# Kernel optimization log

Hardware: AMD Instinct MI355X
Metric: run time of the kernel (lower is better)

The kernel has to match this reference:

```python
import jax, jax.numpy as jnp
import numpy as np

GROUPS = 32
EPS = 1e-6


def group_norm(x, gamma, beta):
    # x: [b, c, d, h, w]
    b, c, d, h, w = x.shape
    xg = x.reshape(b, GROUPS, c // GROUPS, d, h, w)
    mean = xg.mean(axis=(2, 3, 4, 5), keepdims=True)
    var = xg.var(axis=(2, 3, 4, 5), keepdims=True)
    xn = ((xg - mean) * jax.lax.rsqrt(var + EPS)).reshape(b, c, d, h, w)
    return xn * gamma[None, :, None, None, None] + beta[None, :, None, None, None]


def conv1x1(x, w, bias):
    # 1x1x1 Conv3d == channel matmul. x: [b,c,d,h,w], w: [out,in]
    return jnp.einsum('bcdhw,oc->bodhw', x, w) + bias[None, :, None, None, None]


def setup_inputs() -> dict:
    key = jax.random.key(0)
    ks = jax.random.split(key, 6)
    C = 256
    x = jax.random.normal(ks[0], (4, C, 16, 16, 16), dtype=jnp.float32)
    s = 1.0 / np.sqrt(C)
    return {
        'x': x,
        'gn_gamma': jnp.ones((C,), jnp.float32),
        'gn_beta': jnp.zeros((C,), jnp.float32),
        'wq': jax.random.normal(ks[1], (C, C), jnp.float32) * s,
        'bq': jnp.zeros((C,), jnp.float32),
        'wk': jax.random.normal(ks[2], (C, C), jnp.float32) * s,
        'bk': jnp.zeros((C,), jnp.float32),
        'wv': jax.random.normal(ks[3], (C, C), jnp.float32) * s,
        'bv': jnp.zeros((C,), jnp.float32),
        'wo': jax.random.normal(ks[4], (C, C), jnp.float32) * s,
        'bo': jnp.zeros((C,), jnp.float32),
    }


def reference(x, gn_gamma, gn_beta, wq, bq, wk, bk, wv, bv, wo, bo):
    b, c, d, h, w = x.shape
    n = d * h * w
    hn = group_norm(x, gn_gamma, gn_beta)
    q = conv1x1(hn, wq, bq).reshape(b, c, n)  # [b,c,n]
    k = conv1x1(hn, wk, bk).reshape(b, c, n)
    v = conv1x1(hn, wv, bv).reshape(b, c, n)
    # NOTE: no 1/sqrt(c) scaling, faithful to source
    scores = jnp.einsum('bci,bcj->bij', q, k)          # [b,n,n]
    attn = jax.nn.softmax(scores, axis=-1)
    out = jnp.einsum('bij,bcj->bci', attn, v)           # [b,c,n]
    out = out.reshape(b, c, d, h, w)
    out = conv1x1(out, wo, bo)
    return x + out
```

## Files before the change

### kernel.cpp

```cpp
#include <hip/hip_runtime.h>
#include <hip/hip_bf16.h>

#define C_ 256
#define N_ 4096
#define B_ 4
#define NG_ 32
#define CPG_ 8
#define SPLITS 4
#define GPARTS 8
#define JT_PER (N_ / 32 / SPLITS)

typedef _Float16 f16;
typedef __attribute__((ext_vector_type(8))) _Float16 f16v8;
typedef __attribute__((ext_vector_type(2))) __fp16 fp16v2;
typedef __attribute__((ext_vector_type(4))) float f32x4;
typedef __attribute__((ext_vector_type(2))) unsigned int u32x2;
typedef __attribute__((ext_vector_type(4))) unsigned int u32x4;

__device__ __forceinline__ f16v8 ldh(const f16* p) {
    return *reinterpret_cast<const f16v8*>(p);
}
__device__ __forceinline__ f32x4 mfma16(f16v8 a, f16v8 b, f32x4 c) {
    return __builtin_amdgcn_mfma_f32_16x16x32_f16(a, b, c, 0, 0, 0);
}
__device__ __forceinline__ unsigned int pkh(float a, float b) {
    fp16v2 t = __builtin_amdgcn_cvt_pkrtz(a, b);
    return __builtin_bit_cast(unsigned int, t);
}
__device__ __forceinline__ u32x2 plchain(unsigned int x, unsigned int y) {
    u32x2 t = __builtin_amdgcn_permlane32_swap(x, y, false, false);
    return __builtin_amdgcn_permlane16_swap(t.x, t.y, false, false);
}

__global__ __launch_bounds__(256) void conv_w_kernel(
    const float* __restrict__ wq, const float* __restrict__ wk,
    const float* __restrict__ wv, const float* __restrict__ wo,
    f16* __restrict__ wq16, f16* __restrict__ wk16,
    f16* __restrict__ wv16, f16* __restrict__ wo16)
{
    int idx = blockIdx.x * 256 + threadIdx.x;
    wq16[idx] = (f16)wq[idx];
    wk16[idx] = (f16)wk[idx];
    wv16[idx] = (f16)wv[idx];
    wo16[idx] = (f16)wo[idx];
}

__global__ __launch_bounds__(256) void gn_stats_kernel(
    const float* __restrict__ x, float2* __restrict__ psums)
{
    int idx = blockIdx.x;
    int part = idx & (GPARTS - 1);
    int bg = idx >> 3;
    const float4* xv = (const float4*)(x + (size_t)bg * (CPG_ * N_)
                                         + (size_t)part * (CPG_ * N_ / GPARTS));
    int tid = threadIdx.x;
    float s = 0.f, s2 = 0.f;
    #pragma unroll
    for (int i = 0; i < CPG_ * N_ / GPARTS / 4 / 256; i++) {
        float4 v = xv[i * 256 + tid];
        s  += v.x + v.y + v.z + v.w;
        s2 += v.x * v.x + v.y * v.y + v.z * v.z + v.w * v.w;
    }
    #pragma unroll
    for (int off = 32; off > 0; off >>= 1) {
        s  += __shfl_down(s, off);
        s2 += __shfl_down(s2, off);
    }
    __shared__ float rs[4], rs2[4];
    if ((tid & 63) == 0) { rs[tid >> 6] = s; rs2[tid >> 6] = s2; }
    __syncthreads();
    if (tid == 0)
        psums[idx] = make_float2(rs[0] + rs[1] + rs[2] + rs[3],
                                 rs2[0] + rs2[1] + rs2[2] + rs2[3]);
}

__global__ __launch_bounds__(256) void gn_apply_kernel(
    const float* __restrict__ x, const float2* __restrict__ psums,
    const float* __restrict__ gamma, const float* __restrict__ beta,
    f16* __restrict__ hn)
{
    int idx = blockIdx.x;
    int p2 = idx & 15;
    int bg = idx >> 4;
    int b = bg >> 5, g = bg & 31;
    float S = 0.f, S2 = 0.f;
    #pragma unroll
    for (int s = 0; s < GPARTS; s++) {
        float2 ps = psums[bg * GPARTS + s];
        S += ps.x; S2 += ps.y;
    }
    float mean = S / (float)(CPG_ * N_);
    float rstd = rsqrtf(S2 / (float)(CPG_ * N_) - mean * mean + 1e-6f);
    int i = p2 * 256 + threadIdx.x;
    const float* xp = x + (size_t)(b * C_ + g * CPG_) * N_;
    f16v8 H;
    #pragma unroll
    for (int cc = 0; cc < CPG_; cc++) {
        float ga = gamma[g * CPG_ + cc] * rstd;
        float be = beta[g * CPG_ + cc];
        H[cc] = (f16)((xp[(size_t)cc * N_ + i] - mean) * ga + be);
    }
    *reinterpret_cast<f16v8*>(hn + (size_t)(b * N_ + i) * C_ + g * CPG_) = H;
}

__global__ __launch_bounds__(256) void proj_qk_kernel(
    const f16* __restrict__ hn, const f16* __restrict__ wq16,
    const f16* __restrict__ wk16, const float* __restrict__ bq,
    const float* __restrict__ bk, f16* __restrict__ qo, f16* __restrict__ ko)
{
    int it = blockIdx.x, b = blockIdx.y, z = blockIdx.z;
    int which = z >> 1, ochalf = z & 1;
    const f16* wgt = which ? wk16 : wq16;
    const float* bias = which ? bk : bq;
    f16* outp = which ? ko : qo;
    int tid = threadIdx.x, w = tid >> 6, l = tid & 63;
    int l15 = l & 15, lhi = l >> 4;
    int i0 = it * 64 + w * 16;
    size_t arow = (size_t)(b * N_ + i0 + l15) * C_ + lhi * 8;
    f16v8 af[8];
    #pragma unroll
    for (int kk = 0; kk < 8; kk++) af[kk] = ldh(hn + arow + kk * 32);
    for (int oc = ochalf * 8; oc < ochalf * 8 + 8; oc++) {
        f32x4 acc = {0.f, 0.f, 0.f, 0.f};
        size_t wrow = (size_t)(oc * 16 + l15) * C_ + lhi * 8;
        #pragma unroll
        for (int kk = 0; kk < 8; kk++)
            acc = mfma16(af[kk], ldh(wgt + wrow + kk * 32), acc);
        float bia = bias[oc * 16 + l15];
        #pragma unroll
        for (int r = 0; r < 4; r++)
            outp[(size_t)(b * N_ + i0 + lhi * 4 + r) * C_ + oc * 16 + l15] =
                (f16)(acc[r] + bia);
    }
}

__global__ __launch_bounds__(256) void proj_v_kernel(
    const f16* __restrict__ hn, const f16* __restrict__ wv16,
    const float* __restrict__ bv, f16* __restrict__ vT)
{
    int it = blockIdx.x, b = blockIdx.y;
    int tid = threadIdx.x, w = tid >> 6, l = tid & 63;
    int l15 = l & 15, lhi = l >> 4;
    int o0 = w * 64, i0 = it * 32;
    f32x4 acc[4][2];
    #pragma unroll
    for (int mc = 0; mc < 4; mc++)
        #pragma unroll
        for (int nc = 0; nc < 2; nc++) acc[mc][nc] = (f32x4){0.f, 0.f, 0.f, 0.f};
    for (int kk = 0; kk < 8; kk++) {
        f16v8 af[4], bfv[2];
        #pragma unroll
        for (int mc = 0; mc < 4; mc++)
            af[mc] = ldh(wv16 + (size_t)(o0 + mc * 16 + l15) * C_ + kk * 32 + lhi * 8);
        #pragma unroll
        for (int nc = 0; nc < 2; nc++)
            bfv[nc] = ldh(hn + (size_t)(b * N_ + i0 + nc * 16 + l15) * C_ + kk * 32 + lhi * 8);
        #pragma unroll
        for (int mc = 0; mc < 4; mc++)
            #pragma unroll
            for (int nc = 0; nc < 2; nc++)
                acc[mc][nc] = mfma16(af[mc], bfv[nc], acc[mc][nc]);
    }
    #pragma unroll
    for (int mc = 0; mc < 4; mc++) {
        float bia[4];
        #pragma unroll
        for (int r = 0; r < 4; r++) bia[r] = bv[o0 + mc * 16 + lhi * 4 + r];
        #pragma unroll
        for (int nc = 0; nc < 2; nc++)
            #pragma unroll
            for (int r = 0; r < 4; r++) {
                int o = o0 + mc * 16 + lhi * 4 + r;
                int i = i0 + nc * 16 + l15;
                vT[(size_t)(b * C_ + o) * N_ + i] = (f16)(acc[mc][nc][r] + bia[r]);
            }
    }
}

__device__ __forceinline__ void stage_k(const f16* kbase, f16* dst, int j0,
                                        int w, int l) {
    #pragma unroll
    for (int rd = 0; rd < 4; rd++) {
        int cb = (rd * 4 + w) * 64;
        int mc = cb + l;
        int row = mc >> 5;
        int xoff = ((mc & 31) << 4) ^ ((row & 7) << 4);
        const f16* gsrc = kbase + (size_t)(j0 + row) * C_ + (xoff >> 1);
        __builtin_amdgcn_global_load_lds(
            (const __attribute__((address_space(1))) void*)gsrc,
            (__attribute__((address_space(3))) void*)(dst + (size_t)cb * 8),
            16, 0, 0);
    }
}
__device__ __forceinline__ void stage_v(const f16* vbase, f16* dst, int j0,
                                        int w, int l) {
    int tid = w * 64 + l;
    int colu = ((l & 3) ^ ((l >> 3) & 3)) * 8;
    #pragma unroll
    for (int s = 0; s < 4; s++) {
        int cb = s * 256 + w * 64;
        const f16* gsrc = vbase + (size_t)(s * 64 + (tid >> 2)) * N_ + j0 + colu;
        __builtin_amdgcn_global_load_lds(
            (const __attribute__((address_space(1))) void*)gsrc,
            (__attribute__((address_space(3))) void*)(dst + (size_t)cb * 8),
            16, 0, 0);
    }
}

__global__ __launch_bounds__(256, 2) void flash_split_kernel(
    const f16* __restrict__ q, const f16* __restrict__ k,
    const f16* __restrict__ vT,
    f16* __restrict__ o0p, f16* __restrict__ o1p,
    f16* __restrict__ o2p, f16* __restrict__ o3p,
    float2* __restrict__ stats)
{
    int bi = blockIdx.x;
    int g = bi & 15;
    int it = bi >> 4;
    int b = g >> 2, split = g & 3;
    int tid = threadIdx.x, w = tid >> 6, l = tid & 63;
    int l15 = l & 15, lhi = l >> 4;
    int i0 = it * 128 + w * 32;
    int jt0 = split * JT_PER;
    __shared__ __align__(16) f16 kb[32][256];
    __shared__ __align__(16) f16 vb[2][256][32];

    const f16* kbase = k + (size_t)b * N_ * C_;
    const f16* vbase = vT + (size_t)b * C_ * N_;

    f16v8 qfA[8], qfB_[8];
    {
        size_t qrow0 = (size_t)(b * N_ + i0 + l15) * C_ + lhi * 8;
        size_t qrow1 = (size_t)(b * N_ + i0 + 16 + l15) * C_ + lhi * 8;
        #pragma unroll
        for (int kk = 0; kk < 8; kk++) {
            qfA[kk]  = ldh(q + qrow0 + kk * 32);
            qfB_[kk] = ldh(q + qrow1 + kk * 32);
        }
    }

    f32x4 oaccA[16], oaccB[16];
    #pragma unroll
    for (int cc = 0; cc < 16; cc++) {
        oaccA[cc] = (f32x4){0.f, 0.f, 0.f, 0.f};
        oaccB[cc] = (f32x4){0.f, 0.f, 0.f, 0.f};
    }
    float mA = -1e30f, rsA = 0.f;
    float mB = -1e30f, rsB = 0.f;

    int lhiV = lhi ^ ((l15 >> 1) & 3);

    stage_k(kbase, &kb[0][0], jt0 * 32, w, l);
    stage_v(vbase, &vb[0][0][0], jt0 * 32, w, l);
    __syncthreads();

    for (int jt = 0; jt < JT_PER; jt++) {
        int cur = jt & 1;
        int j0 = (jt0 + jt) * 32;

        if (jt + 1 < JT_PER)
            stage_v(vbase, &vb[cur ^ 1][0][0], j0 + 32, w, l);

        const char* kbc = (const char*)&kb[0][0];
        f32x4 sA0 = {0.f,0.f,0.f,0.f}, sA1 = {0.f,0.f,0.f,0.f};
        f32x4 sB0 = {0.f,0.f,0.f,0.f}, sB1 = {0.f,0.f,0.f,0.f};
        __builtin_amdgcn_s_setprio(1);
        #pragma unroll
        for (int kk = 0; kk < 8; kk++) {
            int row0 = l15, row1 = 16 + l15;
            int off0 = row0 * 512 + ((kk * 64 + lhi * 16) ^ ((row0 & 7) << 4));
            int off1 = row1 * 512 + ((kk * 64 + lhi * 16) ^ ((row1 & 7) << 4));
            f16v8 kf0 = *reinterpret_cast<const f16v8*>(kbc + off0);
            f16v8 kf1 = *reinterpret_cast<const f16v8*>(kbc + off1);
            sA0 = mfma16(kf0, qfA[kk], sA0);
            sA1 = mfma16(kf1, qfA[kk], sA1);
            sB0 = mfma16(kf0, qfB_[kk], sB0);
            sB1 = mfma16(kf1, qfB_[kk], sB1);
        }
        __builtin_amdgcn_s_setprio(0);

        __syncthreads();

        if (jt + 1 < JT_PER)
            stage_k(kbase, &kb[0][0], j0 + 32, w, l);

        float mtA = fmaxf(fmaxf(fmaxf(sA0[0], sA0[1]), fmaxf(sA0[2], sA0[3])),
                          fmaxf(fmaxf(sA1[0], sA1[1]), fmaxf(sA1[2], sA1[3])));
        float mtB = fmaxf(fmaxf(fmaxf(sB0[0], sB0[1]), fmaxf(sB0[2], sB0[3])),
                          fmaxf(fmaxf(sB1[0], sB1[1]), fmaxf(sB1[2], sB1[3])));
        mtA = fmaxf(mtA, __shfl_xor(mtA, 16));
        mtA = fmaxf(mtA, __shfl_xor(mtA, 32));
        mtB = fmaxf(mtB, __shfl_xor(mtB, 16));
        mtB = fmaxf(mtB, __shfl_xor(mtB, 32));
        if (!__all(mtA <= mA + 8.f && mtB <= mB + 8.f)) {
            float mnA = fmaxf(mA, mtA), mnB = fmaxf(mB, mtB);
            float scA = __expf(mA - mnA), scB = __expf(mB - mnB);
            mA = mnA; mB = mnB;
            rsA *= scA; rsB *= scB;
            #pragma unroll
            for (int cc = 0; cc < 16; cc++) {
                #pragma unroll
                for (int r = 0; r < 4; r++) {
                    oaccA[cc][r] *= scA;
                    oaccB[cc][r] *= scB;
                }
            }
        }
        float pA0[4], pA1[4], pB0[4], pB1[4];
        float lsA = 0.f, lsB = 0.f;
        #pragma unroll
        for (int r = 0; r < 4; r++) {
            pA0[r] = __expf(sA0[r] - mA);
            pA1[r] = __expf(sA1[r] - mA);
            pB0[r] = __expf(sB0[r] - mB);
            pB1[r] = __expf(sB1[r] - mB);
            lsA += pA0[r] + pA1[r];
            lsB += pB0[r] + pB1[r];
        }
        rsA += lsA; rsB += lsB;

        u32x2 rA01 = plchain(pkh(pA0[0], pA0[1]), pkh(pA1[0], pA1[1]));
        u32x2 rA23 = plchain(pkh(pA0[2], pA0[3]), pkh(pA1[2], pA1[3]));
        u32x4 fA = {rA01.x, rA23.x, rA01.y, rA23.y};
        f16v8 pfA = __builtin_bit_cast(f16v8, fA);
        u32x2 rB01 = plchain(pkh(pB0[0], pB0[1]), pkh(pB1[0], pB1[1]));
        u32x2 rB23 = plchain(pkh(pB0[2], pB0[3]), pkh(pB1[2], pB1[3]));
        u32x4 fB = {rB01.x, rB23.x, rB01.y, rB23.y};
        f16v8 pfB = __builtin_bit_cast(f16v8, fB);

        const f16* vbc = &vb[cur][0][0];
        __builtin_amdgcn_s_setprio(1);
        #pragma unroll
        for (int cc = 0; cc < 16; cc++) {
            f16v8 vf = ldh(vbc + (cc * 16 + l15) * 32 + lhiV * 8);
            oaccA[cc] = mfma16(vf, pfA, oaccA[cc]);
            oaccB[cc] = mfma16(vf, pfB, oaccB[cc]);
        }
        __builtin_amdgcn_s_setprio(0);

        __syncthreads();
    }

    rsA += __shfl_xor(rsA, 16); rsA += __shfl_xor(rsA, 32);
    rsB += __shfl_xor(rsB, 16); rsB += __shfl_xor(rsB, 32);
    float invA = 1.f / rsA, invB = 1.f / rsB;

    f16* op = (split == 0) ? o0p : (split == 1) ? o1p : (split == 2) ? o2p : o3p;
    size_t obaseA = (size_t)(b * N_ + i0 + l15) * C_;
    size_t obaseB = (size_t)(b * N_ + i0 + 16 + l15) * C_;
    #pragma unroll
    for (int cc = 0; cc < 16; cc++) {
        uint2 stA = {pkh(oaccA[cc][0] * invA, oaccA[cc][1] * invA),
                     pkh(oaccA[cc][2] * invA, oaccA[cc][3] * invA)};
        uint2 stB = {pkh(oaccB[cc][0] * invB, oaccB[cc][1] * invB),
                     pkh(oaccB[cc][2] * invB, oaccB[cc][3] * invB)};
        *reinterpret_cast<uint2*>(op + obaseA + cc * 16 + lhi * 4) = stA;
        *reinterpret_cast<uint2*>(op + obaseB + cc * 16 + lhi * 4) = stB;
    }
    if (lhi == 0) {
        stats[((size_t)split * B_ + b) * N_ + i0 + l15]      = make_float2(mA, rsA);
        stats[((size_t)split * B_ + b) * N_ + i0 + 16 + l15] = make_float2(mB, rsB);
    }
}

__global__ __launch_bounds__(256) void combine_kernel(
    const f16* __restrict__ o0p, const f16* __restrict__ o1p,
    const f16* __restrict__ o2p, const f16* __restrict__ o3p,
    const float2* __restrict__ stats, f16* __restrict__ att)
{
    int idx = blockIdx.x * 256 + threadIdx.x;
    int rowg = idx >> 5;
    int cof = (idx & 31) * 8;
    float2 st[SPLITS];
    float M = -1e30f;
    #pragma unroll
    for (int s = 0; s < SPLITS; s++) {
        st[s] = stats[(size_t)s * B_ * N_ + rowg];
        M = fmaxf(M, st[s].x);
    }
    float a[SPLITS], L = 0.f;
    #pragma unroll
    for (int s = 0; s < SPLITS; s++) {
        a[s] = st[s].y * __expf(st[s].x - M);
        L += a[s];
    }
    float inv = 1.f / L;
    size_t base = (size_t)rowg * C_ + cof;
    f16v8 v0 = ldh(o0p + base), v1 = ldh(o1p + base);
    f16v8 v2 = ldh(o2p + base), v3 = ldh(o3p + base);
    f16v8 o = v0 * (f16)(a[0] * inv) + v1 * (f16)(a[1] * inv)
            + v2 * (f16)(a[2] * inv) + v3 * (f16)(a[3] * inv);
    *reinterpret_cast<f16v8*>(att + base) = o;
}

__global__ __launch_bounds__(256) void final_kernel(
    const f16* __restrict__ att, const f16* __restrict__ wo16,
    const float* __restrict__ bo, const float* __restrict__ x,
    float* __restrict__ out)
{
    int bx = blockIdx.x, b = blockIdx.y;
    int it = bx >> 1, half = bx & 1;
    int tid = threadIdx.x, w = tid >> 6, l = tid & 63;
    int l15 = l & 15, lhi = l >> 4;
    int o0 = half * 128 + w * 32, i0 = it * 64;
    f32x4 acc[2][4];
    #pragma unroll
    for (int mc = 0; mc < 2; mc++)
        #pragma unroll
        for (int nc = 0; nc < 4; nc++) acc[mc][nc] = (f32x4){0.f, 0.f, 0.f, 0.f};
    for (int kk = 0; kk < 8; kk++) {
        f16v8 af[2], bfv[4];
        #pragma unroll
        for (int mc = 0; mc < 2; mc++)
            af[mc] = ldh(wo16 + (size_t)(o0 + mc * 16 + l15) * C_ + kk * 32 + lhi * 8);
        #pragma unroll
        for (int nc = 0; nc < 4; nc++)
            bfv[nc] = ldh(att + (size_t)(b * N_ + i0 + nc * 16 + l15) * C_ + kk * 32 + lhi * 8);
        #pragma unroll
        for (int mc = 0; mc < 2; mc++)
            #pragma unroll
            for (int nc = 0; nc < 4; nc++)
                acc[mc][nc] = mfma16(af[mc], bfv[nc], acc[mc][nc]);
    }
    #pragma unroll
    for (int mc = 0; mc < 2; mc++) {
        float bia[4];
        #pragma unroll
        for (int r = 0; r < 4; r++) bia[r] = bo[o0 + mc * 16 + lhi * 4 + r];
        #pragma unroll
        for (int nc = 0; nc < 4; nc++)
            #pragma unroll
            for (int r = 0; r < 4; r++) {
                int o = o0 + mc * 16 + lhi * 4 + r;
                int i = i0 + nc * 16 + l15;
                size_t idx = (size_t)(b * C_ + o) * N_ + i;
                out[idx] = x[idx] + acc[mc][nc][r] + bia[r];
            }
    }
}

extern "C" void kernel_launch(void* const* d_in, const int* in_sizes, int n_in,
                              void* d_out, int out_size, void* d_ws, size_t ws_size,
                              hipStream_t stream) {
    const float* x  = (const float*)d_in[0];
    const float* gg = (const float*)d_in[1];
    const float* gb = (const float*)d_in[2];
    const float* wq = (const float*)d_in[3];
    const float* bq = (const float*)d_in[4];
    const float* wk = (const float*)d_in[5];
    const float* bk = (const float*)d_in[6];
    const float* wv = (const float*)d_in[7];
    const float* bv = (const float*)d_in[8];
    const float* wo = (const float*)d_in[9];
    const float* bo = (const float*)d_in[10];
    float* out = (float*)d_out;

    char* p = (char*)d_ws;
    const size_t WSZ = (size_t)C_ * C_ * 2;
    const size_t HSZ = (size_t)B_ * N_ * C_ * 2;
    const size_t HN  = (size_t)B_ * N_ * C_;
    f16* wq16 = (f16*)p; p += WSZ;
    f16* wk16 = (f16*)p; p += WSZ;
    f16* wv16 = (f16*)p; p += WSZ;
    f16* wo16 = (f16*)p; p += WSZ;
    f16* hn   = (f16*)p; p += HSZ;
    f16* qo   = (f16*)p; p += HSZ;
    f16* ko   = (f16*)p; p += HSZ;
    f16* vt   = (f16*)p; p += HSZ;
    f16* oex  = (f16*)p; p += 3 * HSZ;
    float2* stats = (float2*)p; p += (size_t)SPLITS * B_ * N_ * sizeof(float2);
    float2* psums = (float2*)p; p += (size_t)B_ * NG_ * GPARTS * sizeof(float2);

    f16* o0p = hn;
    f16* o1p = oex;
    f16* o2p = oex + HN;
    f16* o3p = oex + 2 * HN;
    f16* att = qo;

    conv_w_kernel<<<dim3(C_ * C_ / 256), 256, 0, stream>>>(
        wq, wk, wv, wo, wq16, wk16, wv16, wo16);
    gn_stats_kernel<<<dim3(B_ * NG_ * GPARTS), 256, 0, stream>>>(x, psums);
    gn_apply_kernel<<<dim3(B_ * NG_ * 16), 256, 0, stream>>>(
        x, psums, gg, gb, hn);
    proj_qk_kernel<<<dim3(N_ / 64, B_, 4), 256, 0, stream>>>(
        hn, wq16, wk16, bq, bk, qo, ko);
    proj_v_kernel<<<dim3(N_ / 32, B_), 256, 0, stream>>>(hn, wv16, bv, vt);
    flash_split_kernel<<<dim3(N_ / 128 * B_ * SPLITS), 256, 0, stream>>>(
        qo, ko, vt, o0p, o1p, o2p, o3p, stats);
    combine_kernel<<<dim3((int)(HN / 8 / 256)), 256, 0, stream>>>(
        o0p, o1p, o2p, o3p, stats, att);
    final_kernel<<<dim3(N_ / 64 * 2, B_), 256, 0, stream>>>(
        att, wo16, bo, x, out);
}
```

Before: 189.0 us.

## Raise flash-attention KV split count to eight and reuse output buffer for partials

Templates the split-KV flash kernel and combine kernel on the split count and launches eight splits when the workspace is large enough, doubling the grid to improve occupancy across CUs. Partial outputs are placed in the hn buffer, the output tensor (used as scratch before the final kernel overwrites it) and the workspace tail. This frees workspace for more partials. The cost is more partial data written and read in the combine step, and combine now accumulates in fp32.

```diff
diff --git a/kernel.cpp b/kernel.cpp
--- a/kernel.cpp
+++ b/kernel.cpp
@@ -6,9 +6,8 @@
 #define B_ 4
 #define NG_ 32
 #define CPG_ 8
-#define SPLITS 4
 #define GPARTS 8
-#define JT_PER (N_ / 32 / SPLITS)
+#define HN_ ((size_t)B_ * N_ * C_)
 
 typedef _Float16 f16;
 typedef __attribute__((ext_vector_type(8))) _Float16 f16v8;
@@ -30,6 +29,17 @@
 __device__ __forceinline__ u32x2 plchain(unsigned int x, unsigned int y) {
     u32x2 t = __builtin_amdgcn_permlane32_swap(x, y, false, false);
     return __builtin_amdgcn_permlane16_swap(t.x, t.y, false, false);
+}
+__device__ __forceinline__ f16* part_ptr(int s, f16* o0p, f16* od, f16* ows) {
+    return (s == 0) ? o0p
+         : (s <= 2) ? od + (size_t)(s - 1) * HN_
+                    : ows + (size_t)(s - 3) * HN_;
+}
+__device__ __forceinline__ const f16* part_ptr_c(int s, const f16* o0p,
+                                                 const f16* od, const f16* ows) {
+    return (s == 0) ? o0p
+         : (s <= 2) ? od + (size_t)(s - 1) * HN_
+                    : ows + (size_t)(s - 3) * HN_;
 }
 
 __global__ __launch_bounds__(256) void conv_w_kernel(
@@ -207,21 +217,22 @@
     }
 }
 
+template<int NS>
 __global__ __launch_bounds__(256, 2) void flash_split_kernel(
     const f16* __restrict__ q, const f16* __restrict__ k,
     const f16* __restrict__ vT,
-    f16* __restrict__ o0p, f16* __restrict__ o1p,
-    f16* __restrict__ o2p, f16* __restrict__ o3p,
+    f16* __restrict__ o0p, f16* __restrict__ od, f16* __restrict__ ows,
     float2* __restrict__ stats)
 {
+    constexpr int JTP = (N_ / 32) / NS;
     int bi = blockIdx.x;
-    int g = bi & 15;
-    int it = bi >> 4;
-    int b = g >> 2, split = g & 3;
+    int g = bi & (4 * NS - 1);
+    int it = bi / (4 * NS);
+    int b = g / NS, split = g % NS;
     int tid = threadIdx.x, w = tid >> 6, l = tid & 63;
     int l15 = l & 15, lhi = l >> 4;
     int i0 = it * 128 + w * 32;
-    int jt0 = split * JT_PER;
+    int jt0 = split * JTP;
     __shared__ __align__(16) f16 kb[32][256];
     __shared__ __align__(16) f16 vb[2][256][32];
 
@@ -254,11 +265,11 @@
     stage_v(vbase, &vb[0][0][0], jt0 * 32, w, l);
     __syncthreads();
 
-    for (int jt = 0; jt < JT_PER; jt++) {
+    for (int jt = 0; jt < JTP; jt++) {
         int cur = jt & 1;
         int j0 = (jt0 + jt) * 32;
 
-        if (jt + 1 < JT_PER)
+        if (jt + 1 < JTP)
             stage_v(vbase, &vb[cur ^ 1][0][0], j0 + 32, w, l);
 
         const char* kbc = (const char*)&kb[0][0];
@@ -281,7 +292,7 @@
 
         __syncthreads();
 
-        if (jt + 1 < JT_PER)
+        if (jt + 1 < JTP)
             stage_k(kbase, &kb[0][0], j0 + 32, w, l);
 
         float mtA = fmaxf(fmaxf(fmaxf(sA0[0], sA0[1]), fmaxf(sA0[2], sA0[3])),
@@ -345,7 +356,7 @@
     rsB += __shfl_xor(rsB, 16); rsB += __shfl_xor(rsB, 32);
     float invA = 1.f / rsA, invB = 1.f / rsB;
 
-    f16* op = (split == 0) ? o0p : (split == 1) ? o1p : (split == 2) ? o2p : o3p;
+    f16* op = part_ptr(split, o0p, od, ows);
     size_t obaseA = (size_t)(b * N_ + i0 + l15) * C_;
     size_t obaseB = (size_t)(b * N_ + i0 + 16 + l15) * C_;
     #pragma unroll
@@ -363,33 +374,44 @@
     }
 }
 
+template<int NS>
 __global__ __launch_bounds__(256) void combine_kernel(
-    const f16* __restrict__ o0p, const f16* __restrict__ o1p,
-    const f16* __restrict__ o2p, const f16* __restrict__ o3p,
-    const float2* __restrict__ stats, f16* __restrict__ att)
+    const f16* __restrict__ o0p, const f16* __restrict__ od,
+    const f16* __restrict__ ows, const float2* __restrict__ stats,
+    f16* __restrict__ att)
 {
     int idx = blockIdx.x * 256 + threadIdx.x;
     int rowg = idx >> 5;
     int cof = (idx & 31) * 8;
-    float2 st[SPLITS];
+    float2 st[NS];
     float M = -1e30f;
     #pragma unroll
-    for (int s = 0; s < SPLITS; s++) {
+    for (int s = 0; s < NS; s++) {
         st[s] = stats[(size_t)s * B_ * N_ + rowg];
         M = fmaxf(M, st[s].x);
     }
-    float a[SPLITS], L = 0.f;
-    #pragma unroll
-    for (int s = 0; s < SPLITS; s++) {
+    float a[NS], L = 0.f;
+    #pragma unroll
+    for (int s = 0; s < NS; s++) {
         a[s] = st[s].y * __expf(st[s].x - M);
         L += a[s];
     }
     float inv = 1.f / L;
     size_t base = (size_t)rowg * C_ + cof;
-    f16v8 v0 = ldh(o0p + base), v1 = ldh(o1p + base);
-    f16v8 v2 = ldh(o2p + base), v3 = ldh(o3p + base);
-    f16v8 o = v0 * (f16)(a[0] * inv) + v1 * (f16)(a[1] * inv)
-            + v2 * (f16)(a[2] * inv) + v3 * (f16)(a[3] * inv);
+    float acc[8];
+    #pragma unroll
+    for (int e = 0; e < 8; e++) acc[e] = 0.f;
+    #pragma unroll
+    for (int s = 0; s < NS; s++) {
+        const f16* op = part_ptr_c(s, o0p, od, ows);
+        f16v8 v = ldh(op + base);
+        float wgt = a[s] * inv;
+        #pragma unroll
+        for (int e = 0; e < 8; e++) acc[e] += wgt * (float)v[e];
+    }
+    f16v8 o;
+    #pragma unroll
+    for (int e = 0; e < 8; e++) o[e] = (f16)acc[e];
     *reinterpret_cast<f16v8*>(att + base) = o;
 }
 
@@ -457,8 +479,7 @@
 
     char* p = (char*)d_ws;
     const size_t WSZ = (size_t)C_ * C_ * 2;
-    const size_t HSZ = (size_t)B_ * N_ * C_ * 2;
-    const size_t HN  = (size_t)B_ * N_ * C_;
+    const size_t HSZ = HN_ * 2;
     f16* wq16 = (f16*)p; p += WSZ;
     f16* wk16 = (f16*)p; p += WSZ;
     f16* wv16 = (f16*)p; p += WSZ;
@@ -467,14 +488,18 @@
     f16* qo   = (f16*)p; p += HSZ;
     f16* ko   = (f16*)p; p += HSZ;
     f16* vt   = (f16*)p; p += HSZ;
-    f16* oex  = (f16*)p; p += 3 * HSZ;
-    float2* stats = (float2*)p; p += (size_t)SPLITS * B_ * N_ * sizeof(float2);
+    float2* stats = (float2*)p; p += (size_t)8 * B_ * N_ * sizeof(float2);
     float2* psums = (float2*)p; p += (size_t)B_ * NG_ * GPARTS * sizeof(float2);
+    f16* ows = (f16*)p;
+
+    size_t used = (size_t)(p - (char*)d_ws);
+    size_t need8 = used + 5 * HSZ;
+    size_t need4 = used + 1 * HSZ;
+    (void)need4;
+    bool use8 = (ws_size >= need8);
 
     f16* o0p = hn;
-    f16* o1p = oex;
-    f16* o2p = oex + HN;
-    f16* o3p = oex + 2 * HN;
+    f16* od  = (f16*)d_out;
     f16* att = qo;
 
     conv_w_kernel<<<dim3(C_ * C_ / 256), 256, 0, stream>>>(
@@ -485,10 +510,17 @@
     proj_qk_kernel<<<dim3(N_ / 64, B_, 4), 256, 0, stream>>>(
         hn, wq16, wk16, bq, bk, qo, ko);
     proj_v_kernel<<<dim3(N_ / 32, B_), 256, 0, stream>>>(hn, wv16, bv, vt);
-    flash_split_kernel<<<dim3(N_ / 128 * B_ * SPLITS), 256, 0, stream>>>(
-        qo, ko, vt, o0p, o1p, o2p, o3p, stats);
-    combine_kernel<<<dim3((int)(HN / 8 / 256)), 256, 0, stream>>>(
-        o0p, o1p, o2p, o3p, stats, att);
+    if (use8) {
+        flash_split_kernel<8><<<dim3(N_ / 128 * B_ * 8), 256, 0, stream>>>(
+            qo, ko, vt, o0p, od, ows, stats);
+        combine_kernel<8><<<dim3((int)(HN_ / 8 / 256)), 256, 0, stream>>>(
+            o0p, od, ows, stats, att);
+    } else {
+        flash_split_kernel<4><<<dim3(N_ / 128 * B_ * 4), 256, 0, stream>>>(
+            qo, ko, vt, o0p, od, ows, stats);
+        combine_kernel<4><<<dim3((int)(HN_ / 8 / 256)), 256, 0, stream>>>(
+            o0p, od, ows, stats, att);
+    }
     final_kernel<<<dim3(N_ / 64 * 2, B_), 256, 0, stream>>>(
         att, wo16, bo, x, out);
 }
```

New measurement: 204.9 us. +8.4%, slower.
